# Optimization experiments

Measured on AMD Instinct MI355X. Metric: run time of the kernel, lower is better.

The kernel has to match this reference:

```python
import jax, jax.numpy as jnp
import numpy as np

B, H, W, D, HEADS, WS, SHIFT = 64, 28, 28, 384, 12, 7, 3
N = WS * WS  # tokens per window = 49
HEAD_DIM = D // HEADS
SCALE = HEAD_DIM ** -0.5


def _rel_pos_index():
    # standard Swin relative position index, shape [N, N], values in [0, (2*WS-1)^2)
    coords = np.stack(np.meshgrid(np.arange(WS), np.arange(WS), indexing='ij'))  # [2,ws,ws]
    cf = coords.reshape(2, -1)  # [2, N]
    rel = (cf[:, :, None] - cf[:, None, :]).transpose(1, 2, 0).astype(np.int64)  # [N,N,2]
    rel[:, :, 0] += WS - 1
    rel[:, :, 1] += WS - 1
    rel[:, :, 0] *= 2 * WS - 1
    return rel.sum(-1)  # [N, N]


def _attn_mask():
    # shifted-window mask, shape [nW, N, N], entries 0 or -100
    img = np.zeros((H, W))
    cnt = 0
    sl = (slice(0, -WS), slice(-WS, -SHIFT), slice(-SHIFT, None))
    for hs in sl:
        for ws_ in sl:
            img[hs, ws_] = cnt
            cnt += 1
    mw = img.reshape(H // WS, WS, W // WS, WS).transpose(0, 2, 1, 3).reshape(-1, N)  # [nW, N]
    diff = mw[:, None, :] - mw[:, :, None]  # unsqueeze(1) - unsqueeze(2)
    return np.where(diff != 0, -100.0, 0.0).astype(np.float32)


_REL_IDX = _rel_pos_index()
_ATTN_MASK = _attn_mask()


def _ln(x, g, b, eps=1e-5):
    m = x.mean(-1, keepdims=True)
    v = ((x - m) ** 2).mean(-1, keepdims=True)
    return (x - m) * jax.lax.rsqrt(v + eps) * g + b


def _window_partition(x):
    # [B,H,W,C] -> [B*nW, N, C]
    Bz, _, _, C = x.shape
    x = x.reshape(Bz, H // WS, WS, W // WS, WS, C).transpose(0, 1, 3, 2, 4, 5)
    return x.reshape(-1, N, C)


def _window_reverse(xw, Bz):
    # [B*nW, N, C] -> [B,H,W,C]
    C = xw.shape[-1]
    x = xw.reshape(Bz, H // WS, W // WS, WS, WS, C).transpose(0, 1, 3, 2, 4, 5)
    return x.reshape(Bz, H, W, C)


def setup_inputs() -> dict:
    key = jax.random.key(0)
    ks = jax.random.split(key, 12)
    s = 0.02
    return {
        'x': jax.random.normal(ks[0], (B, H * W, D), jnp.float32),
        'norm1_g': jnp.ones((D,), jnp.float32),
        'norm1_b': jnp.zeros((D,), jnp.float32),
        'qkv_w': jax.random.normal(ks[1], (D, 3 * D), jnp.float32) * s,
        'qkv_b': jnp.zeros((3 * D,), jnp.float32),
        'proj_w': jax.random.normal(ks[2], (D, D), jnp.float32) * s,
        'proj_b': jnp.zeros((D,), jnp.float32),
        'rpb_table': jax.random.normal(ks[3], ((2 * WS - 1) ** 2, HEADS), jnp.float32) * s,
        'norm2_g': jnp.ones((D,), jnp.float32),
        'norm2_b': jnp.zeros((D,), jnp.float32),
        'fc1_w': jax.random.normal(ks[4], (D, 4 * D), jnp.float32) * s,
        'fc1_b': jnp.zeros((4 * D,), jnp.float32),
        'fc2_w': jax.random.normal(ks[5], (4 * D, D), jnp.float32) * s,
        'fc2_b': jnp.zeros((D,), jnp.float32),
    }


def reference(x, norm1_g, norm1_b, qkv_w, qkv_b, proj_w, proj_b, rpb_table,
              norm2_g, norm2_b, fc1_w, fc1_b, fc2_w, fc2_b):
    Bz = x.shape[0]
    nW = (H // WS) * (W // WS)
    shortcut = x
    h = _ln(x, norm1_g, norm1_b).reshape(Bz, H, W, D)
    # cyclic shift
    h = jnp.roll(h, shift=(-SHIFT, -SHIFT), axis=(1, 2))
    xw = _window_partition(h)  # [B*nW, N, D]
    # windowed attention
    qkv = (xw @ qkv_w + qkv_b).reshape(-1, N, 3, HEADS, HEAD_DIM)
    q, k, v = [qkv[:, :, i].transpose(0, 2, 1, 3) for i in range(3)]  # [B*nW, H, N, hd]
    attn = jnp.einsum('whnd,whmd->whnm', q * SCALE, k)
    bias = rpb_table[jnp.asarray(_REL_IDX)]  # [N,N,HEADS]
    attn = attn + bias.transpose(2, 0, 1)[None]
    mask = jnp.asarray(_ATTN_MASK)  # [nW,N,N]
    attn = attn.reshape(Bz, nW, HEADS, N, N) + mask[None, :, None]
    attn = jax.nn.softmax(attn.reshape(-1, HEADS, N, N), axis=-1)
    out = jnp.einsum('whnm,whmd->whnd', attn, v)  # [B*nW, H, N, hd]
    out = out.transpose(0, 2, 1, 3).reshape(-1, N, D)
    out = out @ proj_w + proj_b
    # reverse windows + reverse shift
    h = _window_reverse(out, Bz)
    h = jnp.roll(h, shift=(SHIFT, SHIFT), axis=(1, 2)).reshape(Bz, H * W, D)
    x = shortcut + h
    # MLP
    m = _ln(x, norm2_g, norm2_b)
    m = jax.nn.gelu(m @ fc1_w + fc1_b, approximate=False)
    m = m @ fc2_w + fc2_b
    return x + m
```

## Files before the change

kernel.cpp:

```cpp
#include <hip/hip_runtime.h>

typedef unsigned short u16;
typedef unsigned int u32;
typedef __bf16 bf16x8 __attribute__((ext_vector_type(8)));
typedef float f32x4 __attribute__((ext_vector_type(4)));
typedef u32 u32x4 __attribute__((ext_vector_type(4)));

union U8 { u32x4 u; u16 us[8]; bf16x8 bf; };

static __device__ __forceinline__ float b2f(u16 h) {
  union { u32 i; float f; } c; c.i = ((u32)h) << 16; return c.f;
}
static __device__ __forceinline__ u16 f2b(float f) {
  union { float f; u32 i; } c; c.f = f;
  u32 x = c.i;
  return (u16)((x + 0x7fffu + ((x >> 16) & 1u)) >> 16);
}

#define G2LDS16(gp, lp)                                                                   \
  __builtin_amdgcn_global_load_lds((const __attribute__((address_space(1))) void*)(gp),   \
                                   (__attribute__((address_space(3))) void*)(lp), 16, 0, 0)

__global__ __launch_bounds__(256) void wtrans(const float* __restrict__ W, u16* __restrict__ WT,
                                              int K, int N) {
  __shared__ float t[32][33];
  int n0 = blockIdx.x * 32, k0 = blockIdx.y * 32;
  int tx = threadIdx.x, ty = threadIdx.y;
#pragma unroll
  for (int r = 0; r < 4; ++r)
    t[ty + 8 * r][tx] = W[(long)(k0 + ty + 8 * r) * N + n0 + tx];
  __syncthreads();
#pragma unroll
  for (int r = 0; r < 4; ++r)
    WT[(long)(n0 + ty + 8 * r) * K + k0 + tx] = f2b(t[tx][ty + 8 * r]);
}

template<int MODE>
__global__ __launch_bounds__(256) void ln_kernel(const float* __restrict__ src,
                                                 const float* __restrict__ g,
                                                 const float* __restrict__ b,
                                                 u16* __restrict__ dst) {
  int tok = blockIdx.x * 4 + (threadIdx.x >> 6);
  int lane = threadIdx.x & 63;
  long srow;
  if (MODE == 0) {
    int wg = tok / 49, i = tok % 49;
    int bimg = wg >> 4, wloc = wg & 15;
    int wh = wloc >> 2, ww = wloc & 3;
    int ih = i / 7, iw = i % 7;
    int hr = wh * 7 + ih + 3; if (hr >= 28) hr -= 28;
    int wr = ww * 7 + iw + 3; if (wr >= 28) wr -= 28;
    srow = (long)(bimg * 784 + hr * 28 + wr) * 384;
  } else {
    srow = (long)tok * 384;
  }
  const float* p = src + srow + lane * 6;
  float v[6];
#pragma unroll
  for (int t = 0; t < 6; ++t) v[t] = p[t];
  float s = 0.f, ss = 0.f;
#pragma unroll
  for (int t = 0; t < 6; ++t) { s += v[t]; ss += v[t] * v[t]; }
  for (int m = 32; m; m >>= 1) { s += __shfl_xor(s, m); ss += __shfl_xor(ss, m); }
  float mean = s * (1.0f / 384.0f);
  float var  = ss * (1.0f / 384.0f) - mean * mean;
  float rs = rsqrtf(var + 1e-5f);
  u16* o = dst + (long)tok * 384 + lane * 6;
#pragma unroll
  for (int t = 0; t < 6; ++t)
    o[t] = f2b((v[t] - mean) * rs * g[lane * 6 + t] + b[lane * 6 + t]);
}

template<int EPI>
__global__ __launch_bounds__(256, 2) void gemm_big(
    const u16* __restrict__ A, const u16* __restrict__ BT,
    const float* __restrict__ bias, const float* __restrict__ xres,
    u16* __restrict__ Cb, float* __restrict__ Cf, int N, int K) {
  __shared__ __align__(16) u16 As0[128 * 64];
  __shared__ __align__(16) u16 As1[128 * 64];
  __shared__ __align__(16) u16 Bs0[128 * 64];
  __shared__ __align__(16) u16 Bs1[128 * 64];
  const int tid = threadIdx.x;
  const int wave = tid >> 6, lane = tid & 63, quad = lane >> 4, col = lane & 15;

  const int NY = (EPI == 0) ? 9 : (EPI == 1) ? 12 : 3;
  const int nwg = gridDim.x * gridDim.y;
  const int id = blockIdx.x + blockIdx.y * gridDim.x;
  const int sid = (id & 7) * (nwg >> 3) + (id >> 3);
  const int mi = sid / NY, ni = sid - mi * NY;
  const long m0 = (long)mi * 128;
  const int n0 = ni * 128;

  const int rm = (wave & 1) * 64, cn = (wave >> 1) * 64;
  f32x4 acc[4][4];
#pragma unroll
  for (int i = 0; i < 4; ++i)
#pragma unroll
    for (int j = 0; j < 4; ++j) acc[i][j] = f32x4{0.f, 0.f, 0.f, 0.f};

  const int K64 = K >> 6;
  const int sr = lane >> 3;
  const int sc = (lane & 7) ^ sr;
  const u16* gA = A  + (m0 + wave * 32 + sr) * (long)K + sc * 8;
  const u16* gB = BT + ((long)(n0 + wave * 32 + sr)) * K + sc * 8;

#define STAGE(kt, AS, BS)                                                        \
  {                                                                              \
    _Pragma("unroll")                                                            \
    for (int c = 0; c < 4; ++c) {                                                \
      G2LDS16(gA + (long)c * 8 * K + (kt) * 64, &AS[wave * 2048 + c * 512]);     \
      G2LDS16(gB + (long)c * 8 * K + (kt) * 64, &BS[wave * 2048 + c * 512]);     \
    }                                                                            \
  }

#define COMPUTE(AS, BS)                                                          \
  {                                                                              \
    _Pragma("unroll")                                                            \
    for (int kk = 0; kk < 2; ++kk) {                                             \
      U8 af[4], bfr[4];                                                          \
      _Pragma("unroll")                                                          \
      for (int i = 0; i < 4; ++i) {                                              \
        int row = rm + i * 16 + col;                                             \
        int slot = (kk * 4 + quad) ^ (row & 7);                                  \
        af[i].u = *(const u32x4*)&AS[row * 64 + slot * 8];                       \
      }                                                                          \
      _Pragma("unroll")                                                          \
      for (int j = 0; j < 4; ++j) {                                              \
        int row = cn + j * 16 + col;                                             \
        int slot = (kk * 4 + quad) ^ (row & 7);                                  \
        bfr[j].u = *(const u32x4*)&BS[row * 64 + slot * 8];                      \
      }                                                                          \
      _Pragma("unroll")                                                          \
      for (int i = 0; i < 4; ++i)                                                \
        _Pragma("unroll")                                                        \
        for (int j = 0; j < 4; ++j)                                              \
          acc[i][j] = __builtin_amdgcn_mfma_f32_16x16x32_bf16(af[i].bf, bfr[j].bf, acc[i][j], 0, 0, 0); \
    }                                                                            \
  }

  STAGE(0, As0, Bs0);
  __syncthreads();
  for (int kt = 0; kt < K64; kt += 2) {
    if (kt + 1 < K64) STAGE(kt + 1, As1, Bs1);
    COMPUTE(As0, Bs0);
    __syncthreads();
    if (kt + 2 < K64) STAGE(kt + 2, As0, Bs0);
    COMPUTE(As1, Bs1);
    __syncthreads();
  }
#undef STAGE
#undef COMPUTE

#pragma unroll
  for (int j = 0; j < 4; ++j) {
    int n = n0 + cn + j * 16 + col;
    float bv = bias[n];
#pragma unroll
    for (int i = 0; i < 4; ++i) {
#pragma unroll
      for (int rr = 0; rr < 4; ++rr) {
        int row = (int)m0 + rm + i * 16 + quad * 4 + rr;
        float v = acc[i][j][rr] + bv;
        if (EPI == 0) {
          Cb[(long)row * N + n] = f2b(v);
        } else if (EPI == 1) {
          float gl = 0.5f * v * (1.0f + erff(v * 0.70710678118654752f));
          Cb[(long)row * N + n] = f2b(gl);
        } else if (EPI == 2) {
          int wg = row / 49, i49 = row - wg * 49;
          int bimg = wg >> 4, wloc = wg & 15;
          int wh = wloc >> 2, ww = wloc & 3;
          int ih = i49 / 7, iw = i49 - (i49 / 7) * 7;
          int ho = wh * 7 + ih + 3; if (ho >= 28) ho -= 28;
          int wo = ww * 7 + iw + 3; if (wo >= 28) wo -= 28;
          long dst = (long)(bimg * 784 + ho * 28 + wo) * 384 + n;
          Cf[dst] = v + xres[dst];
        } else {
          long idx = (long)row * 384 + n;
          Cf[idx] = v + Cf[idx];
        }
      }
    }
  }
}

__global__ __launch_bounds__(256) void attn_kernel(const u16* __restrict__ qkv,
                                                   const float* __restrict__ rpb,
                                                   u16* __restrict__ obuf) {
  __shared__ __align__(16) float ks[4 * 49 * 32];
  __shared__ __align__(16) float vs[4 * 49 * 32];
  int w = blockIdx.x, h0 = blockIdx.y * 4;
  int wloc = w & 15, wh = wloc >> 2, ww = wloc & 3;

  for (int c = threadIdx.x; c < 1568; c += 256) {
    int kv = (c >= 784) ? 1 : 0;
    int c2 = c - kv * 784;
    int h = c2 / 196, r = c2 - h * 196, j = r >> 2, cc = r & 3;
    U8 t; t.u = *(const u32x4*)(qkv + ((long)w * 49 + j) * 1152 + 384 + kv * 384 + (h0 + h) * 32 + cc * 8);
    float* d = (kv ? vs : ks) + (h * 49 + j) * 32 + cc * 8;
#pragma unroll
    for (int e = 0; e < 8; ++e) d[e] = b2f(t.us[e]);
  }
  __syncthreads();

  int hl = threadIdx.x >> 6, lane = threadIdx.x & 63;
  int head = h0 + hl;
  int i = lane;
  if (lane < 49) {
    const u16* qp = qkv + ((long)w * 49 + i) * 1152 + head * 32;
    float q[32];
#pragma unroll
    for (int t = 0; t < 4; ++t) {
      U8 a; a.u = *(const u32x4*)(qp + t * 8);
#pragma unroll
      for (int e = 0; e < 8; ++e) q[t * 8 + e] = b2f(a.us[e]) * 0.17677669529663689f;
    }
    int ih = i / 7, iw = i % 7;
    int regi = ((wh < 3) ? 0 : ((ih < 4) ? 1 : 2)) * 3 + ((ww < 3) ? 0 : ((iw < 4) ? 1 : 2));
    const float* kbase = ks + hl * 49 * 32;
    const float* vbase = vs + hl * 49 * 32;
    float s[49];
    float mx = -1e30f;
#pragma unroll
    for (int jh = 0; jh < 7; ++jh) {
      int rh = (wh < 3) ? 0 : ((jh < 4) ? 1 : 2);
#pragma unroll
      for (int jw = 0; jw < 7; ++jw) {
        int j = jh * 7 + jw;
        const float* kp = kbase + j * 32;
        float dot = 0.f;
#pragma unroll
        for (int d = 0; d < 32; ++d) dot += q[d] * kp[d];
        int regj = rh * 3 + ((ww < 3) ? 0 : ((jw < 4) ? 1 : 2));
        int idx = (ih - jh + 6) * 13 + (iw - jw + 6);
        float sv = dot + rpb[idx * 12 + head];
        if (regi != regj) sv -= 100.0f;
        s[j] = sv;
        mx = fmaxf(mx, sv);
      }
    }
    float l = 0.f;
#pragma unroll
    for (int j = 0; j < 49; ++j) { s[j] = __expf(s[j] - mx); l += s[j]; }
    float inv = 1.0f / l;
    float oacc[32];
#pragma unroll
    for (int d = 0; d < 32; ++d) oacc[d] = 0.f;
#pragma unroll
    for (int j = 0; j < 49; ++j) {
      float pj = s[j];
      const float* vp = vbase + j * 32;
#pragma unroll
      for (int d = 0; d < 32; ++d) oacc[d] += pj * vp[d];
    }
    u16* op = obuf + ((long)w * 49 + i) * 384 + head * 32;
#pragma unroll
    for (int t = 0; t < 4; ++t) {
      U8 o;
#pragma unroll
      for (int e = 0; e < 8; ++e) o.us[e] = f2b(oacc[t * 8 + e] * inv);
      *(u32x4*)(op + t * 8) = o.u;
    }
  }
}

extern "C" void kernel_launch(void* const* d_in, const int* in_sizes, int n_in,
                              void* d_out, int out_size, void* d_ws, size_t ws_size,
                              hipStream_t stream) {
  const float* x     = (const float*)d_in[0];
  const float* n1g   = (const float*)d_in[1];
  const float* n1b   = (const float*)d_in[2];
  const float* qkvw  = (const float*)d_in[3];
  const float* qkvb  = (const float*)d_in[4];
  const float* projw = (const float*)d_in[5];
  const float* projb = (const float*)d_in[6];
  const float* rpb   = (const float*)d_in[7];
  const float* n2g   = (const float*)d_in[8];
  const float* n2b   = (const float*)d_in[9];
  const float* fc1w  = (const float*)d_in[10];
  const float* fc1b  = (const float*)d_in[11];
  const float* fc2w  = (const float*)d_in[12];
  const float* fc2b  = (const float*)d_in[13];
  float* out = (float*)d_out;

  u16* qkvwT  = (u16*)d_ws;
  u16* projwT = qkvwT + 442368;
  u16* fc1wT  = projwT + 147456;
  u16* fc2wT  = fc1wT + 589824;
  u16* wsA    = fc2wT + 589824;
  u16* wsB    = wsA + 19267584;
  u16* xw   = wsA;
  u16* obuf = wsA;
  u16* abuf = wsA;
  u16* qkvB = wsB;
  u16* midB = wsB;

  wtrans<<<dim3(36, 12), dim3(32, 8), 0, stream>>>(qkvw, qkvwT, 384, 1152);
  wtrans<<<dim3(12, 12), dim3(32, 8), 0, stream>>>(projw, projwT, 384, 384);
  wtrans<<<dim3(48, 12), dim3(32, 8), 0, stream>>>(fc1w, fc1wT, 384, 1536);
  wtrans<<<dim3(12, 48), dim3(32, 8), 0, stream>>>(fc2w, fc2wT, 1536, 384);

  ln_kernel<0><<<12544, 256, 0, stream>>>(x, n1g, n1b, xw);
  gemm_big<0><<<dim3(392, 9), 256, 0, stream>>>(xw, qkvwT, qkvb, nullptr, qkvB, nullptr, 1152, 384);
  attn_kernel<<<dim3(1024, 3), 256, 0, stream>>>(qkvB, rpb, obuf);
  gemm_big<2><<<dim3(392, 3), 256, 0, stream>>>(obuf, projwT, projb, x, nullptr, out, 384, 384);
  ln_kernel<1><<<12544, 256, 0, stream>>>(out, n2g, n2b, abuf);
  gemm_big<1><<<dim3(392, 12), 256, 0, stream>>>(abuf, fc1wT, fc1b, nullptr, midB, nullptr, 1536, 384);
  gemm_big<3><<<dim3(392, 3), 256, 0, stream>>>(midB, fc2wT, fc2b, nullptr, nullptr, out, 384, 1536);
}
```

Before: 635.8 us.

## Use MFMA for window attention with precomputed bias-plus-mask tables

Rewrites the windowed attention kernel so that QK^T and PV run on bf16 MFMA 16x16x32 instructions, replacing the per-thread scalar fp32 dot-product loops. K, V and the probabilities are staged in LDS as bf16. A new small kernel precomputes the combined relative-position bias and shift mask per window type and head into an MFMA-fragment layout, written into the qkv weight workspace after the QKV GEMM has consumed it. The probabilities are now rounded to bf16 before PV, which lowers precision, and the bias table reuses workspace memory, which depends on launch ordering.

```diff
diff --git a/kernel.cpp b/kernel.cpp
--- a/kernel.cpp
+++ b/kernel.cpp
@@ -5,6 +5,7 @@
 typedef __bf16 bf16x8 __attribute__((ext_vector_type(8)));
 typedef float f32x4 __attribute__((ext_vector_type(4)));
 typedef u32 u32x4 __attribute__((ext_vector_type(4)));
+typedef u32 u32x2 __attribute__((ext_vector_type(2)));
 
 union U8 { u32x4 u; u16 us[8]; bf16x8 bf; };
 
@@ -184,84 +185,165 @@
   }
 }
 
+__global__ __launch_bounds__(256) void bmt_kernel(const float* __restrict__ rpb,
+                                                  float* __restrict__ bmt) {
+  int th = blockIdx.y;
+  int type = th / 12, head = th - type * 12;
+  int e = blockIdx.x * 256 + threadIdx.x;
+  int tj = e >> 8, ti = (e >> 6) & 3, quad = (e >> 4) & 3, c = e & 15;
+  int i = ti * 16 + c;
+  int ih = i / 7, iw = i - ih * 7;
+  int regi = ((type & 2) ? ((ih < 4) ? 1 : 2) : 0) * 3 + ((type & 1) ? ((iw < 4) ? 1 : 2) : 0);
+  f32x4 v;
+#pragma unroll
+  for (int r = 0; r < 4; ++r) {
+    int j = tj * 16 + quad * 4 + r;
+    float val = -1e30f;
+    if (i < 49 && j < 49) {
+      int jh = j / 7, jw = j - jh * 7;
+      int idx = (ih - jh + 6) * 13 + (iw - jw + 6);
+      val = rpb[idx * 12 + head];
+      int regj = ((type & 2) ? ((jh < 4) ? 1 : 2) : 0) * 3 + ((type & 1) ? ((jw < 4) ? 1 : 2) : 0);
+      if (regi != regj) val -= 100.0f;
+    }
+    v[r] = val;
+  }
+  ((f32x4*)bmt)[((long)th * 16 + tj * 4 + ti) * 64 + quad * 16 + c] = v;
+}
+
 __global__ __launch_bounds__(256) void attn_kernel(const u16* __restrict__ qkv,
-                                                   const float* __restrict__ rpb,
+                                                   const float* __restrict__ bmt,
                                                    u16* __restrict__ obuf) {
-  __shared__ __align__(16) float ks[4 * 49 * 32];
-  __shared__ __align__(16) float vs[4 * 49 * 32];
-  int w = blockIdx.x, h0 = blockIdx.y * 4;
-  int wloc = w & 15, wh = wloc >> 2, ww = wloc & 3;
-
-  for (int c = threadIdx.x; c < 1568; c += 256) {
-    int kv = (c >= 784) ? 1 : 0;
-    int c2 = c - kv * 784;
-    int h = c2 / 196, r = c2 - h * 196, j = r >> 2, cc = r & 3;
-    U8 t; t.u = *(const u32x4*)(qkv + ((long)w * 49 + j) * 1152 + 384 + kv * 384 + (h0 + h) * 32 + cc * 8);
-    float* d = (kv ? vs : ks) + (h * 49 + j) * 32 + cc * 8;
-#pragma unroll
-    for (int e = 0; e < 8; ++e) d[e] = b2f(t.us[e]);
-  }
+  __shared__ __align__(16) u16 Ks[64 * 136];
+  __shared__ __align__(16) u16 Vs[64 * 130];
+  __shared__ __align__(16) u16 PL[4 * 64 * 72];
+  const int w = blockIdx.x, h0 = blockIdx.y * 4;
+  const int tid = threadIdx.x;
+  const int hl = tid >> 6, lane = tid & 63, quad = lane >> 4, c = lane & 15;
+  const int head = h0 + hl;
+  const int wloc = w & 15;
+  const int type = (((wloc >> 2) == 3) ? 2 : 0) + (((wloc & 3) == 3) ? 1 : 0);
+
+#pragma unroll
+  for (int it = 0; it < 4; ++it) {
+    int cc = tid + it * 256;
+    int j = cc >> 4, ch = cc & 15;
+    u32x4 val = {0u, 0u, 0u, 0u};
+    if (j < 49)
+      val = *(const u32x4*)(qkv + ((long)w * 49 + j) * 1152 + 384 + h0 * 32 + ch * 8);
+    *(u32x4*)&Ks[j * 136 + ch * 8] = val;
+  }
+#pragma unroll
+  for (int it = 0; it < 16; ++it) {
+    int cc = tid + it * 256;
+    int j = cc >> 6, c4 = cc & 63;
+    u32 val = 0u;
+    if (j < 49)
+      val = *(const u32*)(qkv + ((long)w * 49 + j) * 1152 + 768 + h0 * 32 + c4 * 2);
+    *(u32*)&Vs[j * 130 + c4 * 2] = val;
+  }
+
+  U8 qf[4];
+#pragma unroll
+  for (int ti = 0; ti < 4; ++ti)
+    qf[ti].u = *(const u32x4*)(qkv + ((long)w * 49 + ti * 16 + c) * 1152 + head * 32 + quad * 8);
   __syncthreads();
 
-  int hl = threadIdx.x >> 6, lane = threadIdx.x & 63;
-  int head = h0 + hl;
-  int i = lane;
-  if (lane < 49) {
-    const u16* qp = qkv + ((long)w * 49 + i) * 1152 + head * 32;
-    float q[32];
-#pragma unroll
-    for (int t = 0; t < 4; ++t) {
-      U8 a; a.u = *(const u32x4*)(qp + t * 8);
-#pragma unroll
-      for (int e = 0; e < 8; ++e) q[t * 8 + e] = b2f(a.us[e]) * 0.17677669529663689f;
-    }
-    int ih = i / 7, iw = i % 7;
-    int regi = ((wh < 3) ? 0 : ((ih < 4) ? 1 : 2)) * 3 + ((ww < 3) ? 0 : ((iw < 4) ? 1 : 2));
-    const float* kbase = ks + hl * 49 * 32;
-    const float* vbase = vs + hl * 49 * 32;
-    float s[49];
-    float mx = -1e30f;
-#pragma unroll
-    for (int jh = 0; jh < 7; ++jh) {
-      int rh = (wh < 3) ? 0 : ((jh < 4) ? 1 : 2);
-#pragma unroll
-      for (int jw = 0; jw < 7; ++jw) {
-        int j = jh * 7 + jw;
-        const float* kp = kbase + j * 32;
-        float dot = 0.f;
-#pragma unroll
-        for (int d = 0; d < 32; ++d) dot += q[d] * kp[d];
-        int regj = rh * 3 + ((ww < 3) ? 0 : ((jw < 4) ? 1 : 2));
-        int idx = (ih - jh + 6) * 13 + (iw - jw + 6);
-        float sv = dot + rpb[idx * 12 + head];
-        if (regi != regj) sv -= 100.0f;
-        s[j] = sv;
-        mx = fmaxf(mx, sv);
+  U8 kf[4];
+#pragma unroll
+  for (int tj = 0; tj < 4; ++tj)
+    kf[tj].u = *(const u32x4*)&Ks[(tj * 16 + c) * 136 + hl * 32 + quad * 8];
+  f32x4 s[4][4];
+#pragma unroll
+  for (int tj = 0; tj < 4; ++tj)
+#pragma unroll
+    for (int ti = 0; ti < 4; ++ti)
+      s[tj][ti] = __builtin_amdgcn_mfma_f32_16x16x32_bf16(kf[tj].bf, qf[ti].bf,
+                                                          f32x4{0.f, 0.f, 0.f, 0.f}, 0, 0, 0);
+
+  const f32x4* btb = (const f32x4*)bmt + ((long)(type * 12 + head) * 16) * 64 + quad * 16 + c;
+#pragma unroll
+  for (int tj = 0; tj < 4; ++tj)
+#pragma unroll
+    for (int ti = 0; ti < 4; ++ti) {
+      f32x4 bv = btb[(tj * 4 + ti) * 64];
+#pragma unroll
+      for (int r = 0; r < 4; ++r)
+        s[tj][ti][r] = fmaf(s[tj][ti][r], 0.17677669529663689f, bv[r]);
+    }
+
+#pragma unroll
+  for (int ti = 0; ti < 4; ++ti) {
+    float m = -1e30f;
+#pragma unroll
+    for (int tj = 0; tj < 4; ++tj)
+#pragma unroll
+      for (int r = 0; r < 4; ++r) m = fmaxf(m, s[tj][ti][r]);
+    m = fmaxf(m, __shfl_xor(m, 16));
+    m = fmaxf(m, __shfl_xor(m, 32));
+    float l = 0.f;
+#pragma unroll
+    for (int tj = 0; tj < 4; ++tj)
+#pragma unroll
+      for (int r = 0; r < 4; ++r) {
+        float p = __expf(s[tj][ti][r] - m);
+        s[tj][ti][r] = p;
+        l += p;
       }
-    }
-    float l = 0.f;
-#pragma unroll
-    for (int j = 0; j < 49; ++j) { s[j] = __expf(s[j] - mx); l += s[j]; }
+    l += __shfl_xor(l, 16);
+    l += __shfl_xor(l, 32);
     float inv = 1.0f / l;
-    float oacc[32];
-#pragma unroll
-    for (int d = 0; d < 32; ++d) oacc[d] = 0.f;
-#pragma unroll
-    for (int j = 0; j < 49; ++j) {
-      float pj = s[j];
-      const float* vp = vbase + j * 32;
-#pragma unroll
-      for (int d = 0; d < 32; ++d) oacc[d] += pj * vp[d];
-    }
-    u16* op = obuf + ((long)w * 49 + i) * 384 + head * 32;
-#pragma unroll
-    for (int t = 0; t < 4; ++t) {
-      U8 o;
-#pragma unroll
-      for (int e = 0; e < 8; ++e) o.us[e] = f2b(oacc[t * 8 + e] * inv);
-      *(u32x4*)(op + t * 8) = o.u;
-    }
-  }
+#pragma unroll
+    for (int tj = 0; tj < 4; ++tj)
+#pragma unroll
+      for (int r = 0; r < 4; ++r) s[tj][ti][r] *= inv;
+  }
+
+#pragma unroll
+  for (int ti = 0; ti < 4; ++ti)
+#pragma unroll
+    for (int tj = 0; tj < 4; ++tj) {
+      u32 lo = (u32)f2b(s[tj][ti][0]) | ((u32)f2b(s[tj][ti][1]) << 16);
+      u32 hi = (u32)f2b(s[tj][ti][2]) | ((u32)f2b(s[tj][ti][3]) << 16);
+      *(u32x2*)&PL[hl * 4608 + (ti * 16 + c) * 72 + tj * 16 + quad * 4] = u32x2{lo, hi};
+    }
+
+  f32x4 oacc[4][2];
+#pragma unroll
+  for (int t2 = 0; t2 < 4; ++t2) {
+    oacc[t2][0] = f32x4{0.f, 0.f, 0.f, 0.f};
+    oacc[t2][1] = f32x4{0.f, 0.f, 0.f, 0.f};
+  }
+#pragma unroll
+  for (int kk = 0; kk < 2; ++kk) {
+    U8 pa[4];
+#pragma unroll
+    for (int t2 = 0; t2 < 4; ++t2)
+      pa[t2].u = *(const u32x4*)&PL[hl * 4608 + (t2 * 16 + c) * 72 + kk * 32 + quad * 8];
+    U8 vf[2];
+#pragma unroll
+    for (int td = 0; td < 2; ++td)
+#pragma unroll
+      for (int e = 0; e < 8; ++e)
+        vf[td].us[e] = Vs[(kk * 32 + quad * 8 + e) * 130 + hl * 32 + td * 16 + c];
+#pragma unroll
+    for (int t2 = 0; t2 < 4; ++t2)
+#pragma unroll
+      for (int td = 0; td < 2; ++td)
+        oacc[t2][td] = __builtin_amdgcn_mfma_f32_16x16x32_bf16(pa[t2].bf, vf[td].bf, oacc[t2][td], 0, 0, 0);
+  }
+
+#pragma unroll
+  for (int t2 = 0; t2 < 4; ++t2)
+#pragma unroll
+    for (int r = 0; r < 4; ++r) {
+      int i = t2 * 16 + quad * 4 + r;
+      if (i < 49) {
+        u16* op = obuf + ((long)w * 49 + i) * 384 + head * 32 + c;
+        op[0]  = f2b(oacc[t2][0][r]);
+        op[16] = f2b(oacc[t2][1][r]);
+      }
+    }
 }
 
 extern "C" void kernel_launch(void* const* d_in, const int* in_sizes, int n_in,
@@ -294,6 +376,7 @@
   u16* abuf = wsA;
   u16* qkvB = wsB;
   u16* midB = wsB;
+  float* bmtb = (float*)qkvwT;
 
   wtrans<<<dim3(36, 12), dim3(32, 8), 0, stream>>>(qkvw, qkvwT, 384, 1152);
   wtrans<<<dim3(12, 12), dim3(32, 8), 0, stream>>>(projw, projwT, 384, 384);
@@ -302,7 +385,8 @@
 
   ln_kernel<0><<<12544, 256, 0, stream>>>(x, n1g, n1b, xw);
   gemm_big<0><<<dim3(392, 9), 256, 0, stream>>>(xw, qkvwT, qkvb, nullptr, qkvB, nullptr, 1152, 384);
-  attn_kernel<<<dim3(1024, 3), 256, 0, stream>>>(qkvB, rpb, obuf);
+  bmt_kernel<<<dim3(4, 48), 256, 0, stream>>>(rpb, bmtb);
+  attn_kernel<<<dim3(1024, 3), 256, 0, stream>>>(qkvB, bmtb, obuf);
   gemm_big<2><<<dim3(392, 3), 256, 0, stream>>>(obuf, projwT, projb, x, nullptr, out, 384, 384);
   ln_kernel<1><<<12544, 256, 0, stream>>>(out, n2g, n2b, abuf);
   gemm_big<1><<<dim3(392, 12), 256, 0, stream>>>(abuf, fc1wT, fc1b, nullptr, midB, nullptr, 1536, 384);
```

After: 562.5 us. 11.5% less time.
